# Optimization experiments

Measured on AMD Instinct MI355X. Metric: run time of the kernel, lower is better.

## Reference

```python
import jax, jax.numpy as jnp
import numpy as np

MU = 1.0
VUL = 1.0
M = 1.0
ETA = 0.5

BATCH = 256
NBIT = 64
NCLASS = 100
TRAIN_SIZE = 200000


def setup_inputs() -> dict:
    key = jax.random.key(0)
    k1, k2, k3, k4, k5 = jax.random.split(key, 5)
    u = jax.random.normal(k1, (BATCH, NBIT), dtype=jnp.float32)
    labels = jax.random.randint(k2, (BATCH,), 0, NCLASS)
    y = jax.nn.one_hot(labels, NCLASS, dtype=jnp.float32)
    # unique indices into the training-set buffers
    ind = jax.random.permutation(k3, TRAIN_SIZE)[:BATCH]
    U = jax.random.normal(k4, (NBIT, TRAIN_SIZE), dtype=jnp.float32)
    buf_labels = jax.random.randint(k5, (TRAIN_SIZE,), 0, NCLASS)
    Y = jax.nn.one_hot(buf_labels, NCLASS, dtype=jnp.float32).T  # (nclass, train_size)
    C = jnp.sign(jax.random.normal(jax.random.fold_in(key, 7), (NBIT, NCLASS), dtype=jnp.float32))
    return {"u": u, "y": y, "ind": ind, "U": U, "Y": Y, "C": C}


def _discrete_center(C, y, b):
    """Discrete cyclic coordinate descent over class rows. C: (nbit, nclass)."""
    Ct = C.T                      # (nclass, nbit)
    Yt = y.T                      # (nclass, batch)
    Q = Yt @ b.T                  # (nclass, nbit), constant across iterations
    G = Yt @ Yt.T                 # (nclass, nclass) Gram of label rows
    nclass = Ct.shape[0]

    def body(i, Ct):
        w = G[:, i].at[i].set(0.0)          # Y_prime @ v, self row excluded
        colsum = Ct.sum(axis=0) - Ct[i]     # C_prime.T @ ones
        new_row = jnp.sign(Q[i] - Ct.T @ w - VUL * colsum)
        return Ct.at[i].set(new_row)

    Ct = jax.lax.fori_loop(0, nclass, body, Ct)
    return Ct.T  # back to (nbit, nclass)


def reference(u, y, ind, U, Y, C):
    yf = y.astype(jnp.float32)
    # persistent buffer updates (detached in the original via .data)
    U_new = U.at[:, ind].set(jax.lax.stop_gradient(u.T))
    Y_new = Y.at[:, ind].set(yf.T)
    # binary targets for this batch
    b = jax.lax.stop_gradient(jnp.sign(MU * (C @ yf.T) + u.T))  # (nbit, batch)
    # DCC update of class centers (runs under no_grad in the original)
    C_new = _discrete_center(jax.lax.stop_gradient(C), jax.lax.stop_gradient(yf), b)
    # pairwise similarity loss against the whole training buffer
    s = (yf @ Y_new > 0).astype(u.dtype)                 # (batch, train_size)
    ip = jnp.clip(u @ U_new * 0.5, -100.0, 50.0)          # (batch, train_size)
    metric_loss = jnp.mean((1.0 - s) * jnp.log1p(jnp.exp(M + ip))
                           + s * jnp.log1p(jnp.exp(M - ip)))
    quantization_loss = jnp.mean((b - u.T) ** 2)
    loss = metric_loss + ETA * quantization_loss
    return loss, C_new
```

## Files before the change

kernel.cpp:

```cpp
#include <hip/hip_runtime.h>
#include <hip/hip_bf16.h>

#define T_TOTAL 200000
#define BATCH 256
#define NBIT 64
#define NCLASS 100
#define TN 128
#define NBLK ((T_TOTAL + TN - 1) / TN)

typedef __attribute__((ext_vector_type(8))) short bf16x8;
typedef __attribute__((ext_vector_type(4))) float f32x4;

#define LOG2E 1.4426950408889634f
#define LN2   0.6931471805599453

__device__ __forceinline__ float sgnf(float v) {
    return (v > 0.f) ? 1.f : ((v < 0.f) ? -1.f : 0.f);
}

__device__ __forceinline__ unsigned int pk2(float a, float b) {
    union { __hip_bfloat162 h2; unsigned int ui; } cv;
    cv.h2 = __float22bfloat162_rn(make_float2(a, b));
    return cv.ui;
}

__device__ __forceinline__ float hw_exp2(float x) {
    float r; asm("v_exp_f32 %0, %1" : "=v"(r) : "v"(x)); return r;
}
__device__ __forceinline__ float hw_log2(float x) {
    float r; asm("v_log_f32 %0, %1" : "=v"(r) : "v"(x)); return r;
}

__global__ __launch_bounds__(256) void prep_kernel(const float* __restrict__ y,
                                                   int* __restrict__ labB) {
    const int gt = threadIdx.x;
    const float4* yp = reinterpret_cast<const float4*>(y + gt * NCLASS);
    int l = 0;
    #pragma unroll
    for (int p = 0; p < 25; ++p) {
        float4 v = yp[p];
        if (v.x > 0.5f) l = p * 4;
        if (v.y > 0.5f) l = p * 4 + 1;
        if (v.z > 0.5f) l = p * 4 + 2;
        if (v.w > 0.5f) l = p * 4 + 3;
    }
    labB[gt] = l;
}

__global__ __launch_bounds__(256, 6) void metric_kernel(const float* __restrict__ u,
                                                        const float* __restrict__ U,
                                                        const float* __restrict__ Y,
                                                        const int* __restrict__ ind,
                                                        const int* __restrict__ labB_g,
                                                        double* __restrict__ partial) {
    __shared__ unsigned short Bt[TN * 64];
    __shared__ int   labT[TN];
    __shared__ int   labB[BATCH];
    __shared__ float wpart[4];

    const int tid = threadIdx.x;
    const long t0 = (long)blockIdx.x * TN;

    labB[tid] = labB_g[tid];

    {
        const float4* Y4 = reinterpret_cast<const float4*>(Y);
        const int cb = blockIdx.x * 32;
        #pragma unroll
        for (int it = 0; it < 13; ++it) {
            int idx = it * 256 + tid;
            if (idx < 3200) {
                int row = idx >> 5;
                int lc4 = idx & 31;
                if (cb + lc4 < 50000) {
                    float4 v = Y4[(long)row * 50000 + cb + lc4];
                    int c = lc4 * 4;
                    if (v.x > 0.5f) labT[c]     = row;
                    if (v.y > 0.5f) labT[c + 1] = row;
                    if (v.z > 0.5f) labT[c + 2] = row;
                    if (v.w > 0.5f) labT[c + 3] = row;
                }
            }
        }
    }

    {
        const int c = tid & 127;
        const int h = tid >> 7;
        const long t = t0 + c;
        const bool ok = (t < (long)T_TOTAL);
        const int sw = (c & 7) << 3;
        #pragma unroll
        for (int m = 0; m < 4; ++m) {
            unsigned int w[4];
            #pragma unroll
            for (int pp = 0; pp < 4; ++pp) {
                const int kk = h * 32 + m * 8 + 2 * pp;
                float v0 = 0.f, v1 = 0.f;
                if (ok) {
                    v0 = U[(long)kk * T_TOTAL + t];
                    v1 = U[(long)(kk + 1) * T_TOTAL + t];
                }
                w[pp] = pk2(v0, v1);
            }
            const int k0 = h * 32 + m * 8;
            *reinterpret_cast<uint4*>(&Bt[c * 64 + (k0 ^ sw)]) = make_uint4(w[0], w[1], w[2], w[3]);
        }
    }
    __syncthreads();
    {
        long c = (long)ind[tid] - t0;
        if (c >= 0 && c < TN) {
            labT[c] = labB[tid];
            const int ci = (int)c;
            const int sw = (ci & 7) << 3;
            #pragma unroll
            for (int m = 0; m < 8; ++m) {
                unsigned int w[4];
                #pragma unroll
                for (int pp = 0; pp < 4; ++pp) {
                    float v0 = u[tid * NBIT + m * 8 + 2 * pp];
                    float v1 = u[tid * NBIT + m * 8 + 2 * pp + 1];
                    w[pp] = pk2(v0, v1);
                }
                *reinterpret_cast<uint4*>(&Bt[ci * 64 + ((m * 8) ^ sw)]) = make_uint4(w[0], w[1], w[2], w[3]);
            }
        }
    }
    __syncthreads();

    const int wid  = tid >> 6;
    const int lane = tid & 63;
    const int lr   = lane & 15;
    const int g4   = lane >> 4;

    bf16x8 afrag[4][2];
    #pragma unroll
    for (int mt = 0; mt < 4; ++mt) {
        #pragma unroll
        for (int kb = 0; kb < 2; ++kb) {
            const int j = wid * 64 + mt * 16 + lr;
            const float* ur = u + j * NBIT + kb * 32 + g4 * 8;
            float4 va = *reinterpret_cast<const float4*>(ur);
            float4 vb = *reinterpret_cast<const float4*>(ur + 4);
            union { bf16x8 v; unsigned int w[4]; } pk;
            pk.w[0] = pk2(0.5f * va.x, 0.5f * va.y);
            pk.w[1] = pk2(0.5f * va.z, 0.5f * va.w);
            pk.w[2] = pk2(0.5f * vb.x, 0.5f * vb.y);
            pk.w[3] = pk2(0.5f * vb.z, 0.5f * vb.w);
            afrag[mt][kb] = pk.v;
        }
    }
    int labR[4][4];
    #pragma unroll
    for (int mt = 0; mt < 4; ++mt)
        #pragma unroll
        for (int e = 0; e < 4; ++e)
            labR[mt][e] = labB[wid * 64 + mt * 16 + g4 * 4 + e];

    float sum2 = 0.f;
    for (int nt = 0; nt < 8; ++nt) {
        if (t0 + nt * 16 >= (long)T_TOTAL) break;
        const int col = nt * 16 + lr;
        const int sw = (col & 7) << 3;
        union { bf16x8 v; uint4 q; } b0, b1;
        b0.q = *reinterpret_cast<const uint4*>(&Bt[col * 64 + ((g4 * 8) ^ sw)]);
        b1.q = *reinterpret_cast<const uint4*>(&Bt[col * 64 + ((32 + g4 * 8) ^ sw)]);
        const int labc = labT[col];
        #pragma unroll
        for (int mt = 0; mt < 4; ++mt) {
            f32x4 acc4 = {0.f, 0.f, 0.f, 0.f};
            acc4 = __builtin_amdgcn_mfma_f32_16x16x32_bf16(afrag[mt][0], b0.v, acc4, 0, 0, 0);
            acc4 = __builtin_amdgcn_mfma_f32_16x16x32_bf16(afrag[mt][1], b1.v, acc4, 0, 0, 0);
            #pragma unroll
            for (int e = 0; e < 4; ++e) {
                float ip = fminf(fmaxf(acc4[e], -100.f), 50.f);
                float z  = (labc == labR[mt][e]) ? -ip : ip;
                float tt = fmaf(z, LOG2E, LOG2E);
                sum2 += hw_log2(1.f + hw_exp2(tt));
            }
        }
    }
    for (int off = 32; off; off >>= 1) sum2 += __shfl_xor(sum2, off);
    if (lane == 0) wpart[wid] = sum2;
    __syncthreads();
    if (tid == 0)
        partial[blockIdx.x] = (double)(wpart[0] + wpart[1] + wpart[2] + wpart[3]) * LN2;
}

__global__ __launch_bounds__(256) void dcc_kernel(const float* __restrict__ u,
                                                  const float* __restrict__ C,
                                                  const int* __restrict__ lab,
                                                  float* __restrict__ out_c,
                                                  float* __restrict__ quant_out) {
    __shared__ float Q[NCLASS][NBIT];
    __shared__ float Ct2[NBIT * NCLASS];
    __shared__ int   labL[BATCH];
    __shared__ float wq[4];

    const int tid = threadIdx.x;
    const int k   = tid & 63;
    const int g   = tid >> 6;

    labL[tid] = lab[tid];
    for (int o = tid; o < NCLASS * NBIT; o += 256) {
        ((float*)Q)[o] = 0.f;
        Ct2[o] = C[o];
    }
    __syncthreads();

    float qloc = 0.f;
    for (int jj = 0; jj < 64; jj += 8) {
        float uu[8]; int lj[8];
        #pragma unroll
        for (int p = 0; p < 8; ++p) {
            int j = g * 64 + jj + p;
            lj[p] = labL[j];
            uu[p] = u[j * NBIT + k];
        }
        #pragma unroll
        for (int p = 0; p < 8; ++p) {
            float b = sgnf(Ct2[k * NCLASS + lj[p]] + uu[p]);
            atomicAdd(&Q[lj[p]][k], b);
            float d = b - uu[p];
            qloc += d * d;
        }
    }
    for (int off = 32; off; off >>= 1) qloc += __shfl_xor(qloc, off);
    if ((tid & 63) == 0) wq[g] = qloc;
    __syncthreads();
    if (tid == 0) quant_out[0] = wq[0] + wq[1] + wq[2] + wq[3];

    if (tid < 64) {
        float total = 0.f;
        for (int i = 0; i < NCLASS; ++i) total += Ct2[k * NCLASS + i];
        float qn = Q[0][k], cn = Ct2[k * NCLASS];
        for (int i = 0; i < NCLASS; ++i) {
            float qc = qn, old = cn;
            if (i + 1 < NCLASS) { qn = Q[i + 1][k]; cn = Ct2[k * NCLASS + i + 1]; }
            float nr = sgnf(qc - (total - old));
            Ct2[k * NCLASS + i] = nr;
            total += nr - old;
        }
    }
    __syncthreads();
    for (int o = tid; o < NCLASS * NBIT; o += 256) out_c[o] = Ct2[o];
}

__global__ __launch_bounds__(256) void fin_kernel(const double* __restrict__ partial,
                                                  const float* __restrict__ quant,
                                                  float* __restrict__ out0) {
    __shared__ double wp[4];
    double s = 0.0;
    for (int i = threadIdx.x; i < NBLK; i += 256) s += partial[i];
    for (int off = 32; off; off >>= 1) s += __shfl_xor(s, off);
    if ((threadIdx.x & 63) == 0) wp[threadIdx.x >> 6] = s;
    __syncthreads();
    if (threadIdx.x == 0) {
        double tot = wp[0] + wp[1] + wp[2] + wp[3];
        out0[0] = (float)(tot / ((double)BATCH * (double)T_TOTAL)
                          + 0.5 * ((double)quant[0] / (double)(BATCH * NBIT)));
    }
}

extern "C" void kernel_launch(void* const* d_in, const int* in_sizes, int n_in,
                              void* d_out, int out_size, void* d_ws, size_t ws_size,
                              hipStream_t stream) {
    const float* u   = (const float*)d_in[0];
    const float* y   = (const float*)d_in[1];
    const int*   ind = (const int*)d_in[2];
    const float* U   = (const float*)d_in[3];
    const float* Y   = (const float*)d_in[4];
    const float* C   = (const float*)d_in[5];
    float* out = (float*)d_out;

    float*  quant   = (float*)d_ws;
    int*    labB    = (int*)((char*)d_ws + 64);
    double* partial = (double*)((char*)d_ws + 2048);

    prep_kernel<<<1, 256, 0, stream>>>(y, labB);
    metric_kernel<<<NBLK, 256, 0, stream>>>(u, U, Y, ind, labB, partial);
    dcc_kernel<<<1, 256, 0, stream>>>(u, C, labB, out + 1, quant);
    fin_kernel<<<1, 256, 0, stream>>>(partial, quant, out);
}
```

Before: 281.0 us.

## Vectorize U tile loads to float4, batch Y loads, change LDS swizzle

```diff
diff --git a/kernel.cpp b/kernel.cpp
--- a/kernel.cpp
+++ b/kernel.cpp
@@ -13,6 +13,8 @@
 
 #define LOG2E 1.4426950408889634f
 #define LN2   0.6931471805599453
+
+#define SW(c) (((c) << 1) & 0x38)
 
 __device__ __forceinline__ float sgnf(float v) {
     return (v > 0.f) ? 1.f : ((v < 0.f) ? -1.f : 0.f);
@@ -47,12 +49,12 @@
     labB[gt] = l;
 }
 
-__global__ __launch_bounds__(256, 6) void metric_kernel(const float* __restrict__ u,
-                                                        const float* __restrict__ U,
-                                                        const float* __restrict__ Y,
-                                                        const int* __restrict__ ind,
-                                                        const int* __restrict__ labB_g,
-                                                        double* __restrict__ partial) {
+__global__ __launch_bounds__(256) void metric_kernel(const float* __restrict__ u,
+                                                     const float* __restrict__ U,
+                                                     const float* __restrict__ Y,
+                                                     const int* __restrict__ ind,
+                                                     const int* __restrict__ labB_g,
+                                                     double* __restrict__ partial) {
     __shared__ unsigned short Bt[TN * 64];
     __shared__ int   labT[TN];
     __shared__ int   labB[BATCH];
@@ -66,45 +68,45 @@
     {
         const float4* Y4 = reinterpret_cast<const float4*>(Y);
         const int cb = blockIdx.x * 32;
+        float4 vv[13];
         #pragma unroll
         for (int it = 0; it < 13; ++it) {
-            int idx = it * 256 + tid;
-            if (idx < 3200) {
-                int row = idx >> 5;
-                int lc4 = idx & 31;
-                if (cb + lc4 < 50000) {
-                    float4 v = Y4[(long)row * 50000 + cb + lc4];
-                    int c = lc4 * 4;
-                    if (v.x > 0.5f) labT[c]     = row;
-                    if (v.y > 0.5f) labT[c + 1] = row;
-                    if (v.z > 0.5f) labT[c + 2] = row;
-                    if (v.w > 0.5f) labT[c + 3] = row;
-                }
-            }
+            const int idx = it * 256 + tid;
+            const int row = idx >> 5, lc4 = idx & 31;
+            const bool okk = (idx < 3200) && (cb + lc4 < 50000);
+            vv[it] = okk ? Y4[(long)row * 50000 + cb + lc4]
+                         : make_float4(0.f, 0.f, 0.f, 0.f);
+        }
+        #pragma unroll
+        for (int it = 0; it < 13; ++it) {
+            const int idx = it * 256 + tid;
+            const int row = idx >> 5, c = (idx & 31) * 4;
+            float4 v = vv[it];
+            if (v.x > 0.5f) labT[c]     = row;
+            if (v.y > 0.5f) labT[c + 1] = row;
+            if (v.z > 0.5f) labT[c + 2] = row;
+            if (v.w > 0.5f) labT[c + 3] = row;
         }
     }
 
     {
-        const int c = tid & 127;
-        const int h = tid >> 7;
-        const long t = t0 + c;
-        const bool ok = (t < (long)T_TOTAL);
-        const int sw = (c & 7) << 3;
-        #pragma unroll
-        for (int m = 0; m < 4; ++m) {
-            unsigned int w[4];
-            #pragma unroll
-            for (int pp = 0; pp < 4; ++pp) {
-                const int kk = h * 32 + m * 8 + 2 * pp;
-                float v0 = 0.f, v1 = 0.f;
-                if (ok) {
-                    v0 = U[(long)kk * T_TOTAL + t];
-                    v1 = U[(long)(kk + 1) * T_TOTAL + t];
-                }
-                w[pp] = pk2(v0, v1);
-            }
-            const int k0 = h * 32 + m * 8;
-            *reinterpret_cast<uint4*>(&Bt[c * 64 + (k0 ^ sw)]) = make_uint4(w[0], w[1], w[2], w[3]);
+        const float4* U4 = reinterpret_cast<const float4*>(U);
+        const int tb4 = (int)(t0 >> 2);
+        #pragma unroll
+        for (int it = 0; it < 8; ++it) {
+            const int q   = it * 256 + tid;
+            const int k   = q >> 5;
+            const int tf4 = q & 31;
+            float4 v = make_float4(0.f, 0.f, 0.f, 0.f);
+            if (t0 + tf4 * 4 < (long)T_TOTAL)
+                v = U4[(long)k * (T_TOTAL / 4) + tb4 + tf4];
+            const unsigned int p01 = pk2(v.x, v.y);
+            const unsigned int p23 = pk2(v.z, v.w);
+            const int c0 = tf4 * 4;
+            Bt[(c0    ) * 64 + (k ^ SW(c0    ))] = (unsigned short)(p01);
+            Bt[(c0 + 1) * 64 + (k ^ SW(c0 + 1))] = (unsigned short)(p01 >> 16);
+            Bt[(c0 + 2) * 64 + (k ^ SW(c0 + 2))] = (unsigned short)(p23);
+            Bt[(c0 + 3) * 64 + (k ^ SW(c0 + 3))] = (unsigned short)(p23 >> 16);
         }
     }
     __syncthreads();
@@ -113,7 +115,7 @@
         if (c >= 0 && c < TN) {
             labT[c] = labB[tid];
             const int ci = (int)c;
-            const int sw = (ci & 7) << 3;
+            const int sw = SW(ci);
             #pragma unroll
             for (int m = 0; m < 8; ++m) {
                 unsigned int w[4];
@@ -162,7 +164,7 @@
     for (int nt = 0; nt < 8; ++nt) {
         if (t0 + nt * 16 >= (long)T_TOTAL) break;
         const int col = nt * 16 + lr;
-        const int sw = (col & 7) << 3;
+        const int sw = SW(col);
         union { bf16x8 v; uint4 q; } b0, b1;
         b0.q = *reinterpret_cast<const uint4*>(&Bt[col * 64 + ((g4 * 8) ^ sw)]);
         b1.q = *reinterpret_cast<const uint4*>(&Bt[col * 64 + ((32 + g4 * 8) ^ sw)]);
```

Measured after the change: 232.9 us. 1.21x faster.
